# Optimization experiments

Measured on AMD Instinct MI355X. Metric: run time of the kernel, lower is better.

Reference implementation:

```python
import jax, jax.numpy as jnp
import numpy as np
import math

B, S, T, D = 8, 2048, 2048, 1024
EPS = 1e-5

def _layernorm(x, g, b):
    m = jnp.mean(x, axis=-1, keepdims=True)
    v = jnp.mean((x - m) ** 2, axis=-1, keepdims=True)
    return (x - m) * jax.lax.rsqrt(v + EPS) * g + b

def setup_inputs() -> dict:
    key = jax.random.key(0)
    ks = jax.random.split(key, 8)
    sc = 1.0 / math.sqrt(D)
    return {
        "X": jax.random.normal(ks[0], (B, S, D), jnp.float32),
        "Y": jax.random.normal(ks[1], (B, T, D), jnp.float32),
        "qs": jax.random.normal(ks[2], (D,), jnp.float32),
        "ks_": jax.random.normal(ks[3], (D,), jnp.float32),
        "vs": jax.random.normal(ks[4], (D,), jnp.float32),
        "Wq": jax.random.normal(ks[5], (D, D), jnp.float32) * sc,
        "bq": jnp.zeros((D,), jnp.float32),
        "g1": jnp.ones((D,), jnp.float32),
        "b1": jnp.zeros((D,), jnp.float32),
        "Wov": jax.random.normal(ks[6], (2 * D, D), jnp.float32) * sc,
        "bov": jnp.zeros((2 * D,), jnp.float32),
        "g2": jnp.ones((D,), jnp.float32),
        "b2": jnp.zeros((D,), jnp.float32),
        "mask": jnp.ones((S, T), jnp.int32),
    }

def reference(X, Y, qs, ks_, vs, Wq, bq, g1, b1, Wov, bov, g2, b2, mask):
    d = X.shape[-1]
    # q = LayerNorm(Linear(X)) * sigmoid(qs)
    q = _layernorm(X @ Wq.T + bq, g1, b1) * jax.nn.sigmoid(qs)
    # k = Y * sigmoid(ks)
    k = Y * jax.nn.sigmoid(ks_)
    # per-channel value gate: ov(sigmoid(vs)) -> sigmoid(a) * tanh(b), shape [d]
    ab = Wov @ jax.nn.sigmoid(vs) + bov
    a, bgate = ab[:d], ab[d:]
    v = Y * (jax.nn.sigmoid(a) * jnp.tanh(bgate))
    # attention scores [B, S, T]
    A = jnp.einsum("bsd,btd->bst", q, k) / math.sqrt(d)
    A = jnp.where(mask == 0, jnp.float32(-jnp.inf), A)
    p = jax.nn.softmax(A, axis=-1)
    out = jnp.einsum("bst,btd->bsd", p, v)
    return _layernorm(X + out, g2, b2)
```

## Files before the change

### kernel.cpp

```cpp
#include <hip/hip_runtime.h>
#include <stdint.h>

typedef unsigned short u16;
typedef __bf16 bf16x8 __attribute__((ext_vector_type(8)));
typedef float f32x4v __attribute__((ext_vector_type(4)));

#define BB 8
#define SS 2048
#define TT 2048
#define DD 1024
#define LN_EPS 1e-5f

__device__ __forceinline__ float sigm(float x){ return 1.f/(1.f+__expf(-x)); }

__device__ __forceinline__ u16 f2bf(float v){
  uint32_t x = __builtin_bit_cast(uint32_t, v);
  uint32_t r = x + 0x7fffu + ((x >> 16) & 1u);
  return (u16)(r >> 16);
}
__device__ __forceinline__ float bf2f(u16 u){
  return __builtin_bit_cast(float, (uint32_t)u << 16);
}

__device__ __forceinline__ void gload16(const void* g, void* l){
  __builtin_amdgcn_global_load_lds((const __attribute__((address_space(1))) unsigned int*)g,
                                   (__attribute__((address_space(3))) unsigned int*)l, 16, 0, 0);
}

__device__ __forceinline__ int xcd_swizzle(int orig, int nwg){
  int q = nwg >> 3, r = nwg & 7;
  int xcd = orig & 7, idx = orig >> 3;
  return (xcd < r ? xcd*(q+1) : r*(q+1) + (xcd-r)*q) + idx;
}

__global__ void prep_small(const float* qs, const float* ks, const float* vs,
                           float* sq, float* sk, float* svs){
  int i = blockIdx.x*blockDim.x + threadIdx.x;
  if (i < DD){ sq[i] = sigm(qs[i]); sk[i] = sigm(ks[i]); svs[i] = sigm(vs[i]); }
}

__global__ __launch_bounds__(256) void prep_sv(const float* __restrict__ Wov, const float* __restrict__ bov,
                        const float* __restrict__ svs, float* __restrict__ sv){
  int d = blockIdx.x, tid = threadIdx.x;
  float a = 0.f, b = 0.f;
  for (int j = tid; j < DD; j += 256){
    float s = svs[j];
    a += Wov[(size_t)d*DD + j]*s;
    b += Wov[(size_t)(d+DD)*DD + j]*s;
  }
  #pragma unroll
  for (int o = 32; o; o >>= 1){ a += __shfl_xor(a,o); b += __shfl_xor(b,o); }
  __shared__ float sa[4], sb[4];
  int lane = tid & 63, w = tid >> 6;
  if (!lane){ sa[w] = a; sb[w] = b; }
  __syncthreads();
  if (tid == 0){
    float A = sa[0]+sa[1]+sa[2]+sa[3] + bov[d];
    float Bv= sb[0]+sb[1]+sb[2]+sb[3] + bov[DD+d];
    sv[d] = sigm(A) * tanhf(Bv);
  }
}

__global__ void f32_to_bf16_k(const float* __restrict__ src, u16* __restrict__ dst, int n){
  for (int i = (blockIdx.x*blockDim.x + threadIdx.x)*4; i < n; i += gridDim.x*blockDim.x*4){
    float4 v = *(const float4*)(src + i);
    ushort4 o; o.x = f2bf(v.x); o.y = f2bf(v.y); o.z = f2bf(v.z); o.w = f2bf(v.w);
    *(ushort4*)(dst + i) = o;
  }
}

__global__ __launch_bounds__(256) void scale_kv_transpose(const float* __restrict__ Y,
                            const float* __restrict__ sk, const float* __restrict__ sv,
                            u16* __restrict__ kbf, u16* __restrict__ vT){
  __shared__ float tile[64][65];
  int tx = threadIdx.x & 15, ty = threadIdx.x >> 4;
  int b = blockIdx.z;
  int t0 = blockIdx.x*64, d0 = blockIdx.y*64;
  const float* Yb = Y + ((size_t)b*TT + t0)*DD + d0;
  u16* kb = kbf + ((size_t)b*TT + t0)*DD + d0;
  float4 s = *(const float4*)(sv + d0 + tx*4);
  float4 k4 = *(const float4*)(sk + d0 + tx*4);
  #pragma unroll
  for (int it = 0; it < 4; ++it){
    int t = ty + it*16;
    float4 y = *(const float4*)(Yb + (size_t)t*DD + tx*4);
    ushort4 ko;
    ko.x = f2bf(y.x*k4.x); ko.y = f2bf(y.y*k4.y); ko.z = f2bf(y.z*k4.z); ko.w = f2bf(y.w*k4.w);
    *(ushort4*)(kb + (size_t)t*DD + tx*4) = ko;
    tile[t][tx*4+0] = y.x*s.x; tile[t][tx*4+1] = y.y*s.y;
    tile[t][tx*4+2] = y.z*s.z; tile[t][tx*4+3] = y.w*s.w;
  }
  __syncthreads();
  u16* ob = vT + ((size_t)b*DD + d0)*TT + t0;
  #pragma unroll
  for (int it = 0; it < 4; ++it){
    int dd = ty + it*16;
    ushort4 o;
    o.x = f2bf(tile[tx*4+0][dd]); o.y = f2bf(tile[tx*4+1][dd]);
    o.z = f2bf(tile[tx*4+2][dd]); o.w = f2bf(tile[tx*4+3][dd]);
    *(ushort4*)(ob + (size_t)dd*TT + tx*4) = o;
  }
}

__global__ __launch_bounds__(256) void mask_pack(const int* __restrict__ mask, uint32_t* __restrict__ m32){
  int idx = blockIdx.x*256 + threadIdx.x;
  const int* mp = mask + ((size_t)(idx >> 6))*TT + (idx & 63)*32;
  uint32_t b = 0;
  #pragma unroll
  for (int j = 0; j < 8; ++j){
    int4 v = *(const int4*)(mp + j*4);
    b |= (uint32_t)(v.x != 0) << (j*4+0);
    b |= (uint32_t)(v.y != 0) << (j*4+1);
    b |= (uint32_t)(v.z != 0) << (j*4+2);
    b |= (uint32_t)(v.w != 0) << (j*4+3);
  }
  m32[idx] = b;
}

template<int OUTMODE>
__global__ __launch_bounds__(512, 1)
void gemm256_bt(const u16* __restrict__ A, const u16* __restrict__ B,
                void* __restrict__ Cv, const float* __restrict__ bias,
                const uint32_t* __restrict__ mpk,
                int K, int lda, int ldb, int ldc,
                size_t sA, size_t sB, size_t sC, int ntx, int ntxty, int nwg)
{
  __shared__ __align__(16) u16 As[2][16384];
  __shared__ __align__(16) u16 Bs[2][16384];
  __shared__ float Lsum[256];
  const int tid = threadIdx.x, lane = tid & 63, w = tid >> 6;
  const int wm = w >> 2, wn = w & 3;
  const int sw = xcd_swizzle(blockIdx.x, nwg);
  const int bz_ = sw / ntxty;
  const int rem = sw - bz_*ntxty;
  const int by = rem / ntx, bx = rem - (rem/ntx)*ntx;
  const size_t bz = bz_;
  const int tM = by*256, tN = bx*256;
  const u16* Ab = A + bz*sA;
  const u16* Bb = B + bz*sB;
  const int NT = K >> 6;

  const int srow  = lane >> 3;
  const int sslot = (lane & 7) ^ srow;
  const int frow  = lane & 15;
  const int fs    = lane >> 4;
  const int fx    = lane & 7;

#define BAR() asm volatile("s_barrier" ::: "memory")
#define WAITV(n) asm volatile("s_waitcnt vmcnt(" #n ")" ::: "memory")

#define STAGE(h) do { \
    const int tau_ = (h) >> 2, typ_ = (h) & 3; \
    const int buf_ = tau_ & 1, hi_ = typ_ >> 1, k0_ = tau_ << 6; \
    const u16* src_; int ld_, t0_; u16* dst_; \
    if ((typ_ & 1) == 0){ src_ = Ab; ld_ = lda; t0_ = tM; dst_ = &As[buf_][hi_*8192]; } \
    else                { src_ = Bb; ld_ = ldb; t0_ = tN; dst_ = &Bs[buf_][hi_*8192]; } \
    _Pragma("unroll") \
    for (int i_ = 0; i_ < 2; ++i_){ \
      const int chunk_ = w*2 + i_; \
      gload16(src_ + (size_t)(t0_ + hi_*128 + chunk_*8 + srow)*ld_ + (k0_ + sslot*8), \
              dst_ + chunk_*512); \
    } } while(0)

#define READA(buf, mh, a) do { \
    _Pragma("unroll") for (int m_ = 0; m_ < 4; ++m_) \
    _Pragma("unroll") for (int ks_ = 0; ks_ < 2; ++ks_) \
      a[m_*2+ks_] = *(const bf16x8*)&As[buf][(wm*128 + (mh)*64 + m_*16 + frow)*64 + ((ks_*4+fs)^fx)*8]; \
  } while(0)
#define READB(buf, nh, b) do { \
    _Pragma("unroll") for (int n_ = 0; n_ < 2; ++n_) \
    _Pragma("unroll") for (int ks_ = 0; ks_ < 2; ++ks_) \
      b[n_*2+ks_] = *(const bf16x8*)&Bs[buf][(wn*64 + (nh)*32 + n_*16 + frow)*64 + ((ks_*4+fs)^fx)*8]; \
  } while(0)
#define QUAD(mh, nh, a, b) do { \
    __builtin_amdgcn_s_setprio(1); \
    _Pragma("unroll") for (int m_ = 0; m_ < 4; ++m_) \
    _Pragma("unroll") for (int n_ = 0; n_ < 2; ++n_) \
    _Pragma("unroll") for (int ks_ = 0; ks_ < 2; ++ks_) \
      acc[(mh)*4+m_][(nh)*2+n_] = __builtin_amdgcn_mfma_f32_16x16x32_bf16( \
          a[m_*2+ks_], b[n_*2+ks_], acc[(mh)*4+m_][(nh)*2+n_], 0, 0, 0); \
    __builtin_amdgcn_s_setprio(0); \
  } while(0)
#define LSUM(mh, a) do { \
    if (OUTMODE == 4 && wn == 0){ \
      _Pragma("unroll") for (int m_ = 0; m_ < 4; ++m_){ \
        acc_l[(mh)*4+m_] = __builtin_amdgcn_mfma_f32_16x16x32_bf16(a[m_*2],   vone, acc_l[(mh)*4+m_], 0, 0, 0); \
        acc_l[(mh)*4+m_] = __builtin_amdgcn_mfma_f32_16x16x32_bf16(a[m_*2+1], vone, acc_l[(mh)*4+m_], 0, 0, 0); \
      } \
    } } while(0)

  f32x4v acc[8][4];
  #pragma unroll
  for (int m = 0; m < 8; ++m)
    #pragma unroll
    for (int n = 0; n < 4; ++n) acc[m][n] = (f32x4v){0.f,0.f,0.f,0.f};

  f32x4v acc_l[8];
  bf16x8 vone;
  #pragma unroll
  for (int m = 0; m < 8; ++m) acc_l[m] = (f32x4v){0.f,0.f,0.f,0.f};
  #pragma unroll
  for (int i = 0; i < 8; ++i) vone[i] = (__bf16)1.0f;

  #pragma unroll
  for (int h = 0; h < 8; ++h) STAGE(h);

  bf16x8 a0[8], a1[8], b0[4], b1[4];

  for (int t = 0; t < NT; ++t){
    const int buf = t & 1;
    const int nx = t + 2;
    if (t == NT-1) { WAITV(0); } else { WAITV(8); }
    BAR();
    READA(buf, 0, a0);
    READB(buf, 0, b0);
    QUAD(0, 0, a0, b0);
    LSUM(0, a0);
    BAR();
    READB(buf, 1, b1);
    QUAD(0, 1, a0, b1);
    BAR();
    READA(buf, 1, a1);
    if (nx < NT){ STAGE(nx*4+1); STAGE(nx*4+3); }
    QUAD(1, 1, a1, b1);
    LSUM(1, a1);
    BAR();
    if (nx < NT){ STAGE(nx*4+0); STAGE(nx*4+2); }
    QUAD(1, 0, a1, b0);
  }

  const int erow = (lane >> 4) * 4;
  const int ecol = lane & 15;

  if (OUTMODE == 4){
    if (wn == 0 && ecol == 0){
      #pragma unroll
      for (int m = 0; m < 8; ++m)
        #pragma unroll
        for (int r = 0; r < 4; ++r)
          Lsum[wm*128 + m*16 + erow + r] = acc_l[m][r];
    }
    __syncthreads();
  }

  #pragma unroll
  for (int m = 0; m < 8; ++m){
    float li[4];
    if (OUTMODE == 4){
      #pragma unroll
      for (int r = 0; r < 4; ++r) li[r] = 1.f / Lsum[wm*128 + m*16 + erow + r];
    }
    #pragma unroll
    for (int n = 0; n < 4; ++n){
      const int row0 = tM + wm*128 + m*16 + erow;
      const int col  = tN + wn*64  + n*16 + ecol;
      if (OUTMODE == 0){
        float* C = (float*)Cv + bz*sC;
        #pragma unroll
        for (int r = 0; r < 4; ++r) C[(size_t)(row0+r)*ldc + col] = acc[m][n][r];
      } else if (OUTMODE == 4){
        float* C = (float*)Cv + bz*sC;
        #pragma unroll
        for (int r = 0; r < 4; ++r) C[(size_t)(row0+r)*ldc + col] = acc[m][n][r] * li[r];
      } else if (OUTMODE == 3){
        u16* C = (u16*)Cv + bz*sC;
        const int c32 = (tN + wn*64 + n*16) >> 5;
        #pragma unroll
        for (int r = 0; r < 4; ++r){
          const int row = row0 + r;
          const uint32_t mb = mpk[(size_t)row*64 + c32];
          float e = ((mb >> (col & 31)) & 1u) ? __expf(acc[m][n][r]) : 0.f;
          C[(size_t)row*ldc + col] = f2bf(e);
        }
      } else {
        float bv = (OUTMODE == 2) ? bias[col] : 0.f;
        u16* C = (u16*)Cv + bz*sC;
        #pragma unroll
        for (int r = 0; r < 4; ++r) C[(size_t)(row0+r)*ldc + col] = f2bf(acc[m][n][r] + bv);
      }
    }
  }
#undef STAGE
#undef READA
#undef READB
#undef QUAD
#undef LSUM
#undef BAR
#undef WAITV
}

__global__ __launch_bounds__(256) void ln_q(u16* __restrict__ qb, const float* __restrict__ g1,
                     const float* __restrict__ b1, const float* __restrict__ sq){
  const int w = threadIdx.x >> 6, lane = threadIdx.x & 63;
  const size_t r = (size_t)blockIdx.x * 4 + w;
  u16* row = qb + r * DD;
  uint4 v0 = *(const uint4*)(row + lane*16);
  uint4 v1 = *(const uint4*)(row + lane*16 + 8);
  const u16* vp0 = (const u16*)&v0;
  const u16* vp1 = (const u16*)&v1;
  float x[16];
  #pragma unroll
  for (int i = 0; i < 8; ++i){ x[i] = bf2f(vp0[i]); x[8+i] = bf2f(vp1[i]); }
  float s = 0.f, ss = 0.f;
  #pragma unroll
  for (int i = 0; i < 16; ++i){ s += x[i]; ss += x[i]*x[i]; }
  #pragma unroll
  for (int o = 32; o; o >>= 1){ s += __shfl_xor(s,o); ss += __shfl_xor(ss,o); }
  float mean = s * (1.f/DD);
  float var  = ss * (1.f/DD) - mean*mean;
  float rs = rsqrtf(var + LN_EPS);
  uint4 o0, o1;
  u16* op0 = (u16*)&o0; u16* op1 = (u16*)&o1;
  #pragma unroll
  for (int j = 0; j < 4; ++j){
    float4 g = *(const float4*)(g1 + lane*16 + j*4);
    float4 b = *(const float4*)(b1 + lane*16 + j*4);
    float4 q = *(const float4*)(sq + lane*16 + j*4);
    u16* op = (j < 2) ? (op0 + j*4) : (op1 + (j-2)*4);
    op[0] = f2bf(((x[j*4+0]-mean)*rs*g.x + b.x) * q.x * 0.03125f);
    op[1] = f2bf(((x[j*4+1]-mean)*rs*g.y + b.y) * q.y * 0.03125f);
    op[2] = f2bf(((x[j*4+2]-mean)*rs*g.z + b.z) * q.z * 0.03125f);
    op[3] = f2bf(((x[j*4+3]-mean)*rs*g.w + b.w) * q.w * 0.03125f);
  }
  *(uint4*)(row + lane*16) = o0;
  *(uint4*)(row + lane*16 + 8) = o1;
}

__global__ __launch_bounds__(256) void final_ln(const float* __restrict__ X, float* __restrict__ out,
                         const float* __restrict__ g2, const float* __restrict__ b2){
  const int w = threadIdx.x >> 6, lane = threadIdx.x & 63;
  const size_t r = (size_t)blockIdx.x * 4 + w;
  const float* xr = X + r * DD;
  float* orw = out + r * DD;
  float z[16];
  float s = 0.f, ss = 0.f;
  #pragma unroll
  for (int j = 0; j < 4; ++j){
    float4 xv = *(const float4*)(xr + lane*16 + j*4);
    float4 ov = *(const float4*)(orw + lane*16 + j*4);
    z[j*4+0] = xv.x+ov.x; z[j*4+1] = xv.y+ov.y; z[j*4+2] = xv.z+ov.z; z[j*4+3] = xv.w+ov.w;
  }
  #pragma unroll
  for (int i = 0; i < 16; ++i){ s += z[i]; ss += z[i]*z[i]; }
  #pragma unroll
  for (int o = 32; o; o >>= 1){ s += __shfl_xor(s,o); ss += __shfl_xor(ss,o); }
  float mean = s * (1.f/DD);
  float var  = ss * (1.f/DD) - mean*mean;
  float rs = rsqrtf(var + LN_EPS);
  #pragma unroll
  for (int j = 0; j < 4; ++j){
    float4 g = *(const float4*)(g2 + lane*16 + j*4);
    float4 b = *(const float4*)(b2 + lane*16 + j*4);
    float4 o;
    o.x = (z[j*4+0]-mean)*rs*g.x + b.x;
    o.y = (z[j*4+1]-mean)*rs*g.y + b.y;
    o.z = (z[j*4+2]-mean)*rs*g.z + b.z;
    o.w = (z[j*4+3]-mean)*rs*g.w + b.w;
    *(float4*)(orw + lane*16 + j*4) = o;
  }
}

extern "C" void kernel_launch(void* const* d_in, const int* in_sizes, int n_in,
                              void* d_out, int out_size, void* d_ws, size_t ws_size,
                              hipStream_t stream)
{
  const float* X  = (const float*)d_in[0];
  const float* Y  = (const float*)d_in[1];
  const float* qs = (const float*)d_in[2];
  const float* ks = (const float*)d_in[3];
  const float* vs = (const float*)d_in[4];
  const float* Wq = (const float*)d_in[5];
  const float* bq = (const float*)d_in[6];
  const float* g1 = (const float*)d_in[7];
  const float* b1 = (const float*)d_in[8];
  const float* Wov= (const float*)d_in[9];
  const float* bov= (const float*)d_in[10];
  const float* g2 = (const float*)d_in[11];
  const float* b2 = (const float*)d_in[12];
  const int* mask = (const int*)d_in[13];
  float* out = (float*)d_out;
  (void)in_sizes; (void)n_in; (void)out_size;

  char* ws = (char*)d_ws;
  size_t off = 0;
  auto alloc = [&](size_t bytes) -> void* {
    void* p = ws + off; off += (bytes + 255) & ~(size_t)255; return p;
  };
  u16* qbf  = (u16*)alloc((size_t)BB*SS*DD*2);
  u16* kbf  = (u16*)alloc((size_t)BB*TT*DD*2);
  u16* vT   = (u16*)alloc((size_t)BB*DD*TT*2);
  u16* Xbf  = (u16*)alloc((size_t)BB*SS*DD*2);
  u16* Wqbf = (u16*)alloc((size_t)DD*DD*2);
  float* sq  = (float*)alloc(DD*4);
  float* sk  = (float*)alloc(DD*4);
  float* sv  = (float*)alloc(DD*4);
  float* svs = (float*)alloc(DD*4);
  uint32_t* m32 = (uint32_t*)alloc((size_t)SS*64*4);
  u16* Sbuf = (u16*)alloc((size_t)BB*SS*TT*2);

  prep_small<<<4, 256, 0, stream>>>(qs, ks, vs, sq, sk, svs);
  prep_sv<<<DD, 256, 0, stream>>>(Wov, bov, svs, sv);
  f32_to_bf16_k<<<4096, 256, 0, stream>>>(X, Xbf, BB*SS*DD);
  f32_to_bf16_k<<<1024, 256, 0, stream>>>(Wq, Wqbf, DD*DD);
  dim3 tg(TT/64, DD/64, BB);
  scale_kv_transpose<<<tg, 256, 0, stream>>>(Y, sk, sv, kbf, vT);
  mask_pack<<<(SS*64)/256, 256, 0, stream>>>(mask, m32);

  gemm256_bt<2><<<dim3(256), 512, 0, stream>>>(Xbf, Wqbf, qbf, bq, nullptr,
      DD, DD, DD, DD, 0, 0, 0, 4, 256, 256);
  ln_q<<<(BB*SS)/4, 256, 0, stream>>>(qbf, g1, b1, sq);

  gemm256_bt<3><<<dim3(8*8*BB), 512, 0, stream>>>(
      qbf, kbf, Sbuf, nullptr, m32,
      DD, DD, DD, TT,
      (size_t)SS*DD, (size_t)TT*DD, (size_t)SS*TT, 8, 8*8, 8*8*BB);

  gemm256_bt<4><<<dim3(4*8*BB), 512, 0, stream>>>(
      Sbuf, vT, out, nullptr, nullptr,
      TT, TT, TT, DD,
      (size_t)SS*TT, (size_t)DD*TT, (size_t)SS*DD, 4, 4*8, 4*8*BB);

  final_ln<<<(BB*SS)/4, 256, 0, stream>>>(X, out, g2, b2);
}
```

Baseline: 317.4 us.

## Templatize GEMM M-tile and single-buffer LDS to shrink tiles for more workgroups

Makes the GEMM M-tile height a template parameter and uses 128-row tiles for the Q projection and PV GEMMs, doubling the workgroup count so more CUs are busy. It also drops LDS double buffering: each k-step now waits for all loads, computes, then issues the next tile's loads after a barrier. This cuts LDS use, but global loads no longer overlap with MFMA work inside a workgroup, so the kernel relies on other resident waves to hide memory latency.

Result: slower. 386.4 us (+21.7%).

```diff
diff --git a/kernel.cpp b/kernel.cpp
--- a/kernel.cpp
+++ b/kernel.cpp
@@ -117,7 +117,7 @@
   m32[idx] = b;
 }
 
-template<int OUTMODE>
+template<int OUTMODE, int MREP>
 __global__ __launch_bounds__(512, 1)
 void gemm256_bt(const u16* __restrict__ A, const u16* __restrict__ B,
                 void* __restrict__ Cv, const float* __restrict__ bias,
@@ -125,9 +125,11 @@
                 int K, int lda, int ldb, int ldc,
                 size_t sA, size_t sB, size_t sC, int ntx, int ntxty, int nwg)
 {
-  __shared__ __align__(16) u16 As[2][16384];
-  __shared__ __align__(16) u16 Bs[2][16384];
-  __shared__ float Lsum[256];
+  constexpr int BM = MREP * 32;
+  constexpr int MH = MREP / 2;
+  __shared__ __align__(16) u16 As[BM*64];
+  __shared__ __align__(16) u16 Bs[256*64];
+  __shared__ float Lsum[BM];
   const int tid = threadIdx.x, lane = tid & 63, w = tid >> 6;
   const int wm = w >> 2, wn = w & 3;
   const int sw = xcd_swizzle(blockIdx.x, nwg);
@@ -135,7 +137,7 @@
   const int rem = sw - bz_*ntxty;
   const int by = rem / ntx, bx = rem - (rem/ntx)*ntx;
   const size_t bz = bz_;
-  const int tM = by*256, tN = bx*256;
+  const int tM = by*BM, tN = bx*256;
   const u16* Ab = A + bz*sA;
   const u16* Bb = B + bz*sB;
   const int NT = K >> 6;
@@ -147,86 +149,82 @@
   const int fx    = lane & 7;
 
 #define BAR() asm volatile("s_barrier" ::: "memory")
-#define WAITV(n) asm volatile("s_waitcnt vmcnt(" #n ")" ::: "memory")
-
-#define STAGE(h) do { \
-    const int tau_ = (h) >> 2, typ_ = (h) & 3; \
-    const int buf_ = tau_ & 1, hi_ = typ_ >> 1, k0_ = tau_ << 6; \
-    const u16* src_; int ld_, t0_; u16* dst_; \
-    if ((typ_ & 1) == 0){ src_ = Ab; ld_ = lda; t0_ = tM; dst_ = &As[buf_][hi_*8192]; } \
-    else                { src_ = Bb; ld_ = ldb; t0_ = tN; dst_ = &Bs[buf_][hi_*8192]; } \
-    _Pragma("unroll") \
-    for (int i_ = 0; i_ < 2; ++i_){ \
-      const int chunk_ = w*2 + i_; \
-      gload16(src_ + (size_t)(t0_ + hi_*128 + chunk_*8 + srow)*ld_ + (k0_ + sslot*8), \
-              dst_ + chunk_*512); \
-    } } while(0)
-
-#define READA(buf, mh, a) do { \
-    _Pragma("unroll") for (int m_ = 0; m_ < 4; ++m_) \
+#define WAITV0() asm volatile("s_waitcnt vmcnt(0)" ::: "memory")
+
+  auto stage = [&](int t){
+    const int k0 = t << 6;
+    #pragma unroll
+    for (int i = 0; i < BM/64; ++i)
+      gload16(Ab + (size_t)(tM + i*64 + w*8 + srow)*lda + (k0 + sslot*8),
+              &As[(i*64 + w*8)*64]);
+    #pragma unroll
+    for (int i = 0; i < 4; ++i)
+      gload16(Bb + (size_t)(tN + i*64 + w*8 + srow)*ldb + (k0 + sslot*8),
+              &Bs[(i*64 + w*8)*64]);
+  };
+
+#define READA(mh, a) do { \
+    _Pragma("unroll") for (int m_ = 0; m_ < MH; ++m_) \
     _Pragma("unroll") for (int ks_ = 0; ks_ < 2; ++ks_) \
-      a[m_*2+ks_] = *(const bf16x8*)&As[buf][(wm*128 + (mh)*64 + m_*16 + frow)*64 + ((ks_*4+fs)^fx)*8]; \
+      a[m_*2+ks_] = *(const bf16x8*)&As[(wm*(BM/2) + (mh)*(MH*16) + m_*16 + frow)*64 + ((ks_*4+fs)^fx)*8]; \
   } while(0)
-#define READB(buf, nh, b) do { \
+#define READB(nh, b) do { \
     _Pragma("unroll") for (int n_ = 0; n_ < 2; ++n_) \
     _Pragma("unroll") for (int ks_ = 0; ks_ < 2; ++ks_) \
-      b[n_*2+ks_] = *(const bf16x8*)&Bs[buf][(wn*64 + (nh)*32 + n_*16 + frow)*64 + ((ks_*4+fs)^fx)*8]; \
+      b[n_*2+ks_] = *(const bf16x8*)&Bs[(wn*64 + (nh)*32 + n_*16 + frow)*64 + ((ks_*4+fs)^fx)*8]; \
   } while(0)
 #define QUAD(mh, nh, a, b) do { \
     __builtin_amdgcn_s_setprio(1); \
-    _Pragma("unroll") for (int m_ = 0; m_ < 4; ++m_) \
+    _Pragma("unroll") for (int m_ = 0; m_ < MH; ++m_) \
     _Pragma("unroll") for (int n_ = 0; n_ < 2; ++n_) \
     _Pragma("unroll") for (int ks_ = 0; ks_ < 2; ++ks_) \
-      acc[(mh)*4+m_][(nh)*2+n_] = __builtin_amdgcn_mfma_f32_16x16x32_bf16( \
-          a[m_*2+ks_], b[n_*2+ks_], acc[(mh)*4+m_][(nh)*2+n_], 0, 0, 0); \
+      acc[(mh)*MH+m_][(nh)*2+n_] = __builtin_amdgcn_mfma_f32_16x16x32_bf16( \
+          a[m_*2+ks_], b[n_*2+ks_], acc[(mh)*MH+m_][(nh)*2+n_], 0, 0, 0); \
     __builtin_amdgcn_s_setprio(0); \
   } while(0)
 #define LSUM(mh, a) do { \
     if (OUTMODE == 4 && wn == 0){ \
-      _Pragma("unroll") for (int m_ = 0; m_ < 4; ++m_){ \
-        acc_l[(mh)*4+m_] = __builtin_amdgcn_mfma_f32_16x16x32_bf16(a[m_*2],   vone, acc_l[(mh)*4+m_], 0, 0, 0); \
-        acc_l[(mh)*4+m_] = __builtin_amdgcn_mfma_f32_16x16x32_bf16(a[m_*2+1], vone, acc_l[(mh)*4+m_], 0, 0, 0); \
+      _Pragma("unroll") for (int m_ = 0; m_ < MH; ++m_){ \
+        acc_l[(mh)*MH+m_] = __builtin_amdgcn_mfma_f32_16x16x32_bf16(a[m_*2],   vone, acc_l[(mh)*MH+m_], 0, 0, 0); \
+        acc_l[(mh)*MH+m_] = __builtin_amdgcn_mfma_f32_16x16x32_bf16(a[m_*2+1], vone, acc_l[(mh)*MH+m_], 0, 0, 0); \
       } \
     } } while(0)
 
-  f32x4v acc[8][4];
-  #pragma unroll
-  for (int m = 0; m < 8; ++m)
+  f32x4v acc[MREP][4];
+  #pragma unroll
+  for (int m = 0; m < MREP; ++m)
     #pragma unroll
     for (int n = 0; n < 4; ++n) acc[m][n] = (f32x4v){0.f,0.f,0.f,0.f};
 
-  f32x4v acc_l[8];
+  f32x4v acc_l[MREP];
   bf16x8 vone;
   #pragma unroll
-  for (int m = 0; m < 8; ++m) acc_l[m] = (f32x4v){0.f,0.f,0.f,0.f};
+  for (int m = 0; m < MREP; ++m) acc_l[m] = (f32x4v){0.f,0.f,0.f,0.f};
   #pragma unroll
   for (int i = 0; i < 8; ++i) vone[i] = (__bf16)1.0f;
 
-  #pragma unroll
-  for (int h = 0; h < 8; ++h) STAGE(h);
-
-  bf16x8 a0[8], a1[8], b0[4], b1[4];
+  stage(0);
+
+  bf16x8 a0[MREP], a1[MREP], b0[4], b1[4];
 
   for (int t = 0; t < NT; ++t){
-    const int buf = t & 1;
-    const int nx = t + 2;
-    if (t == NT-1) { WAITV(0); } else { WAITV(8); }
+    WAITV0();
     BAR();
-    READA(buf, 0, a0);
-    READB(buf, 0, b0);
+    READA(0, a0);
+    READB(0, b0);
     QUAD(0, 0, a0, b0);
     LSUM(0, a0);
     BAR();
-    READB(buf, 1, b1);
+    READB(1, b1);
     QUAD(0, 1, a0, b1);
     BAR();
-    READA(buf, 1, a1);
-    if (nx < NT){ STAGE(nx*4+1); STAGE(nx*4+3); }
+    READA(1, a1);
     QUAD(1, 1, a1, b1);
     LSUM(1, a1);
     BAR();
-    if (nx < NT){ STAGE(nx*4+0); STAGE(nx*4+2); }
     QUAD(1, 0, a1, b0);
+    BAR();
+    if (t+1 < NT) stage(t+1);
   }
 
   const int erow = (lane >> 4) * 4;
@@ -235,24 +233,24 @@
   if (OUTMODE == 4){
     if (wn == 0 && ecol == 0){
       #pragma unroll
-      for (int m = 0; m < 8; ++m)
+      for (int m = 0; m < MREP; ++m)
         #pragma unroll
         for (int r = 0; r < 4; ++r)
-          Lsum[wm*128 + m*16 + erow + r] = acc_l[m][r];
+          Lsum[wm*(BM/2) + m*16 + erow + r] = acc_l[m][r];
     }
     __syncthreads();
   }
 
   #pragma unroll
-  for (int m = 0; m < 8; ++m){
+  for (int m = 0; m < MREP; ++m){
     float li[4];
     if (OUTMODE == 4){
       #pragma unroll
-      for (int r = 0; r < 4; ++r) li[r] = 1.f / Lsum[wm*128 + m*16 + erow + r];
+      for (int r = 0; r < 4; ++r) li[r] = 1.f / Lsum[wm*(BM/2) + m*16 + erow + r];
     }
     #pragma unroll
     for (int n = 0; n < 4; ++n){
-      const int row0 = tM + wm*128 + m*16 + erow;
+      const int row0 = tM + wm*(BM/2) + m*16 + erow;
       const int col  = tN + wn*64  + n*16 + ecol;
       if (OUTMODE == 0){
         float* C = (float*)Cv + bz*sC;
@@ -280,13 +278,12 @@
       }
     }
   }
-#undef STAGE
 #undef READA
 #undef READB
 #undef QUAD
 #undef LSUM
 #undef BAR
-#undef WAITV
+#undef WAITV0
 }
 
 __global__ __launch_bounds__(256) void ln_q(u16* __restrict__ qb, const float* __restrict__ g1,
@@ -406,19 +403,19 @@
   scale_kv_transpose<<<tg, 256, 0, stream>>>(Y, sk, sv, kbf, vT);
   mask_pack<<<(SS*64)/256, 256, 0, stream>>>(mask, m32);
 
-  gemm256_bt<2><<<dim3(256), 512, 0, stream>>>(Xbf, Wqbf, qbf, bq, nullptr,
-      DD, DD, DD, DD, 0, 0, 0, 4, 256, 256);
+  gemm256_bt<2,4><<<dim3(512), 512, 0, stream>>>(Xbf, Wqbf, qbf, bq, nullptr,
+      DD, DD, DD, DD, 0, 0, 0, 4, 512, 512);
   ln_q<<<(BB*SS)/4, 256, 0, stream>>>(qbf, g1, b1, sq);
 
-  gemm256_bt<3><<<dim3(8*8*BB), 512, 0, stream>>>(
+  gemm256_bt<3,8><<<dim3(512), 512, 0, stream>>>(
       qbf, kbf, Sbuf, nullptr, m32,
       DD, DD, DD, TT,
-      (size_t)SS*DD, (size_t)TT*DD, (size_t)SS*TT, 8, 8*8, 8*8*BB);
-
-  gemm256_bt<4><<<dim3(4*8*BB), 512, 0, stream>>>(
+      (size_t)SS*DD, (size_t)TT*DD, (size_t)SS*TT, 8, 64, 512);
+
+  gemm256_bt<4,4><<<dim3(512), 512, 0, stream>>>(
       Sbuf, vT, out, nullptr, nullptr,
       TT, TT, TT, DD,
-      (size_t)SS*TT, (size_t)DD*TT, (size_t)SS*DD, 4, 4*8, 4*8*BB);
+      (size_t)SS*TT, (size_t)DD*TT, (size_t)SS*DD, 4, 64, 512);
 
   final_ln<<<(BB*SS)/4, 256, 0, stream>>>(X, out, g2, b2);
 }
```
